# Performance work log

Hardware: AMD Instinct MI355X
Metric: run time of the kernel (lower is better)

The kernel has to match this reference:

```python
import jax, jax.numpy as jnp
import numpy as np

B, MAXLEN, H, T, NC = 2048, 1000, 512, 21, 10  # T = 21 one-hot classes -> seq_len


def _uniform(key, shape, bound):
    return jax.random.uniform(key, shape, jnp.float32, -bound, bound)


def setup_inputs() -> dict:
    key = jax.random.key(0)
    ks = jax.random.split(key, 16)
    k = 1.0 / np.sqrt(H)
    inp = {
        "x": jax.random.randint(ks[0], (B, MAXLEN), 0, 21),
        # layer 0: input size MAXLEN; stacked over 2 directions
        "w_ih0": _uniform(ks[1], (2, 4 * H, MAXLEN), k),
        "w_hh0": _uniform(ks[2], (2, 4 * H, H), k),
        "b_ih0": _uniform(ks[3], (2, 4 * H), k),
        "b_hh0": _uniform(ks[4], (2, 4 * H), k),
        # layer 1: input size 2H
        "w_ih1": _uniform(ks[5], (2, 4 * H, 2 * H), k),
        "w_hh1": _uniform(ks[6], (2, 4 * H, H), k),
        "b_ih1": _uniform(ks[7], (2, 4 * H), k),
        "b_hh1": _uniform(ks[8], (2, 4 * H), k),
        # emb: Linear(21 -> 1) over the seq axis
        "emb_w": _uniform(ks[9], (1, T), 1.0 / np.sqrt(T)),
        "emb_b": _uniform(ks[10], (1,), 1.0 / np.sqrt(T)),
        # fc: Linear(2H -> NC)
        "fc_w": _uniform(ks[11], (NC, 2 * H), 1.0 / np.sqrt(2 * H)),
        "fc_b": _uniform(ks[12], (NC,), 1.0 / np.sqrt(2 * H)),
    }
    return inp


def _lstm_dir(xs, w_ih, w_hh, b_ih, b_hh, reverse):
    # xs: [T, B, I]; PyTorch gate order i, f, g, o
    gx = jnp.einsum('tbi,gi->tbg', xs, w_ih) + b_ih + b_hh  # [T,B,4H]
    h_dim = w_hh.shape[1]
    bsz = xs.shape[1]

    def step(carry, g_t):
        h, c = carry
        g = g_t + h @ w_hh.T
        i, f, gg, o = jnp.split(g, 4, axis=-1)
        c = jax.nn.sigmoid(f) * c + jax.nn.sigmoid(i) * jnp.tanh(gg)
        h = jax.nn.sigmoid(o) * jnp.tanh(c)
        return (h, c), h

    init = (jnp.zeros((bsz, h_dim), xs.dtype), jnp.zeros((bsz, h_dim), xs.dtype))
    _, hs = jax.lax.scan(step, init, gx, reverse=reverse)
    return hs  # [T,B,H], time-aligned (matches torch bidirectional output)


def _bilstm_layer(xs, w_ih, w_hh, b_ih, b_hh):
    hf = _lstm_dir(xs, w_ih[0], w_hh[0], b_ih[0], b_hh[0], reverse=False)
    hb = _lstm_dir(xs, w_ih[1], w_hh[1], b_ih[1], b_hh[1], reverse=True)
    return jnp.concatenate([hf, hb], axis=-1)  # [T,B,2H]


def reference(x, w_ih0, w_hh0, b_ih0, b_hh0, w_ih1, w_hh1, b_ih1, b_hh1,
              emb_w, emb_b, fc_w, fc_b):
    xoh = jax.nn.one_hot(x, 21, dtype=jnp.float32)       # [B, MAXLEN, 21]
    seq = xoh.transpose(2, 0, 1)                          # [T=21, B, MAXLEN]
    seq = _bilstm_layer(seq, w_ih0, w_hh0, b_ih0, b_hh0)  # [T,B,2H]
    seq = _bilstm_layer(seq, w_ih1, w_hh1, b_ih1, b_hh1)  # [T,B,2H]
    # emb: Linear(21->1) applied along seq axis, then squeeze -> [B, 2H]
    z = jnp.einsum('tbh,t->bh', seq, emb_w[0]) + emb_b[0]
    return z @ fc_w.T + fc_b                              # [B, NC]
```

## Files before the change

### kernel.cpp

```cpp
#include <hip/hip_runtime.h>
#include <hip/hip_bf16.h>
#include <cstdint>
#include <cstddef>

#define B_SZ    2048
#define H_SZ    512
#define G4      2048
#define TSTEPS  21
#define MAXLEN  1000
#define KIN     1024
#define NCLS    10

#define BM    128
#define BN    128
#define BKS   32
#define LDSKS 40
#define NITS  16
#define NITG  32
#define GP2   68
#define STEPBUF (3 * BM * LDSKS)
#define GXBUF   (2 * BM * LDSKS)
#define SMEM_BYTES 61440

typedef short bf16x8 __attribute__((ext_vector_type(8)));
typedef float f32x4  __attribute__((ext_vector_type(4)));
typedef unsigned short ushort8 __attribute__((ext_vector_type(8)));

__device__ __forceinline__ unsigned short f2bf(float f) {
  __hip_bfloat16 h = __float2bfloat16(f);
  unsigned short u; __builtin_memcpy(&u, &h, sizeof(u)); return u;
}
__device__ __forceinline__ float bf2f(unsigned short u) {
  __hip_bfloat16 h; __builtin_memcpy(&h, &u, sizeof(h)); return __bfloat162float(h);
}
__device__ __forceinline__ float sigmoidf_(float x) {
  x = fminf(fmaxf(x, -30.f), 30.f);
  return 1.f / (1.f + __expf(-x));
}
__device__ __forceinline__ float tanhf_(float x) {
  float xc = fminf(fmaxf(x, -15.f), 15.f);
  float e = __expf(2.f * xc);
  return (e - 1.f) / (e + 1.f);
}
__device__ __forceinline__ void bar_lgkm() {
  asm volatile("s_waitcnt lgkmcnt(0)" ::: "memory");
  __builtin_amdgcn_s_barrier();
  __builtin_amdgcn_sched_barrier(0);
}
__device__ __forceinline__ int rbase_of(int p) { return (p & 3) * H_SZ + (p >> 2); }

__global__ void prep_rec_kernel(const float* __restrict__ w_hh,
                                unsigned short* __restrict__ Bhi,
                                unsigned short* __restrict__ Blo) {
  size_t idx = (size_t)blockIdx.x * blockDim.x + threadIdx.x;
  const size_t total = (size_t)2 * G4 * H_SZ;
  if (idx >= total) return;
  int k  = (int)(idx % H_SZ);
  size_t rowidx = idx / H_SZ;
  int p  = (int)(rowidx % G4);
  int dd = (int)(rowidx / G4);
  float w = w_hh[((size_t)dd * G4 + rbase_of(p)) * H_SZ + k];
  unsigned short h = f2bf(w);
  Bhi[idx] = h;
  Blo[idx] = f2bf(w - bf2f(h));
}

__global__ void prep_in0_kernel(const float* __restrict__ w_ih0,
                                unsigned short* __restrict__ Bin0) {
  size_t idx = (size_t)blockIdx.x * blockDim.x + threadIdx.x;
  const size_t total = (size_t)2 * G4 * KIN;
  if (idx >= total) return;
  int k  = (int)(idx % KIN);
  size_t rowidx = idx / KIN;
  int p  = (int)(rowidx % G4);
  int dd = (int)(rowidx / G4);
  float v = (k < MAXLEN) ? w_ih0[((size_t)dd * G4 + rbase_of(p)) * MAXLEN + k] : 0.f;
  Bin0[idx] = f2bf(v);
}

__global__ void prep_in1_kernel(const float* __restrict__ w_ih1,
                                unsigned short* __restrict__ Bin1) {
  size_t idx = (size_t)blockIdx.x * blockDim.x + threadIdx.x;
  const size_t total = (size_t)2 * G4 * KIN;
  if (idx >= total) return;
  int k  = (int)(idx % KIN);
  size_t rowidx = idx / KIN;
  int p  = (int)(rowidx % G4);
  int dd = (int)(rowidx / G4);
  Bin1[idx] = f2bf(w_ih1[((size_t)dd * G4 + rbase_of(p)) * KIN + k]);
}

__global__ void prep_b_kernel(const float* __restrict__ b_ih0,
                              const float* __restrict__ b_hh0,
                              const float* __restrict__ b_ih1,
                              const float* __restrict__ b_hh1,
                              float* __restrict__ bias0,
                              float* __restrict__ bias1) {
  int idx = blockIdx.x * blockDim.x + threadIdx.x;
  if (idx >= 2 * G4) return;
  int p  = idx % G4;
  int dd = idx / G4;
  int src = dd * G4 + rbase_of(p);
  bias0[idx] = b_ih0[src] + b_hh0[src];
  bias1[idx] = b_ih1[src] + b_hh1[src];
}

__global__ void prep_x_kernel(const int* __restrict__ x,
                              unsigned int* __restrict__ bits) {
  int idx = blockIdx.x * blockDim.x + threadIdx.x;
  if (idx >= B_SZ * 32) return;
  int b = idx >> 5;
  int w = idx & 31;
  const int* xr = x + (size_t)b * MAXLEN + w * 32;
  int xv[32];
#pragma unroll
  for (int j = 0; j < 32; ++j) {
    int k = w * 32 + j;
    xv[j] = (k < MAXLEN) ? xr[j] : -1;
  }
#pragma unroll
  for (int t = 0; t < TSTEPS; ++t) {
    unsigned int m = 0;
#pragma unroll
    for (int j = 0; j < 32; ++j)
      m |= (xv[j] == t) ? (1u << j) : 0u;
    bits[((size_t)t * B_SZ + b) * 32 + w] = m;
  }
}

template <int LAYER>
__device__ void step_role(char* smraw, int sid, int step,
                          const unsigned short* __restrict__ Bhrec,
                          const unsigned short* __restrict__ Blrec,
                          const float* __restrict__ bias,
                          const unsigned short* __restrict__ h_in,
                          unsigned short* __restrict__ h_out,
                          float* __restrict__ c_st,
                          unsigned short* __restrict__ seq_out,
                          float* __restrict__ zacc,
                          const float* __restrict__ emb_w,
                          const float* __restrict__ gxcur) {
  unsigned short* buf0 = (unsigned short*)smraw;
  unsigned short* buf1 = buf0 + STEPBUF;
  float*          gc   = (float*)smraw;

  const int tid  = threadIdx.x;
  const int lane = tid & 63;
  const int wave = tid >> 6;
  const int wr   = wave >> 1;
  const int wc   = wave & 1;
  const int q    = lane >> 4;
  const int r16  = lane & 15;

  const int xcd  = sid & 7;
  const int slot = sid >> 3;
  const int nb   = xcd * 2 + (slot & 1);
  const int mb   = (slot >> 1) & 15;
  const int d    = slot >> 5;
  const int tcur = d ? (TSTEPS - 1 - step) : step;
  const int n0   = nb * BN;
  const int m0   = mb * BM;

  const unsigned short* Bh_mat = Bhrec + (size_t)d * G4 * H_SZ;
  const unsigned short* Bl_mat = Blrec + (size_t)d * G4 * H_SZ;
  const unsigned short* Ah     = h_in + (size_t)d * B_SZ * H_SZ;

  float bval[4];
#pragma unroll
  for (int nt = 0; nt < 4; ++nt)
    bval[nt] = bias[d * G4 + n0 + wc * 64 + nt * 16 + r16];

  f32x4 acc[2][4];
#pragma unroll
  for (int mt = 0; mt < 2; ++mt)
#pragma unroll
    for (int nt = 0; nt < 4; ++nt) {
      f32x4 z = {0.f, 0.f, 0.f, 0.f};
      acc[mt][nt] = z;
    }

  const int rstg = tid >> 2;
  const int ostg = (tid & 3) * 8;

  ushort8 pbhA, pblA, pvaA, pbhB, pblB, pvaB;
  auto loadA = [&](int kt) {
    const int k0 = kt * BKS;
    pbhA = *(const ushort8*)(Bh_mat + (size_t)(n0 + rstg) * H_SZ + k0 + ostg);
    pblA = *(const ushort8*)(Bl_mat + (size_t)(n0 + rstg) * H_SZ + k0 + ostg);
    pvaA = *(const ushort8*)(Ah + (size_t)(m0 + rstg) * H_SZ + k0 + ostg);
  };
  auto loadB = [&](int kt) {
    const int k0 = kt * BKS;
    pbhB = *(const ushort8*)(Bh_mat + (size_t)(n0 + rstg) * H_SZ + k0 + ostg);
    pblB = *(const ushort8*)(Bl_mat + (size_t)(n0 + rstg) * H_SZ + k0 + ostg);
    pvaB = *(const ushort8*)(Ah + (size_t)(m0 + rstg) * H_SZ + k0 + ostg);
  };
  auto storeA = [&](unsigned short* sA) {
    *(ushort8*)(sA + rstg * LDSKS + ostg)                  = pvaA;
    *(ushort8*)(sA + BM * LDSKS + rstg * LDSKS + ostg)     = pbhA;
    *(ushort8*)(sA + 2 * BM * LDSKS + rstg * LDSKS + ostg) = pblA;
  };
  auto storeB = [&](unsigned short* sA) {
    *(ushort8*)(sA + rstg * LDSKS + ostg)                  = pvaB;
    *(ushort8*)(sA + BM * LDSKS + rstg * LDSKS + ostg)     = pbhB;
    *(ushort8*)(sA + 2 * BM * LDSKS + rstg * LDSKS + ostg) = pblB;
  };
  auto compute = [&](const unsigned short* sA) {
    const unsigned short* sBh = sA + BM * LDSKS;
    const unsigned short* sBl = sBh + BM * LDSKS;
    bf16x8 af[2], bh[4];
#pragma unroll
    for (int mt = 0; mt < 2; ++mt)
      af[mt] = *(const bf16x8*)(sA + (wr * 32 + mt * 16 + r16) * LDSKS + q * 8);
#pragma unroll
    for (int nt = 0; nt < 4; ++nt)
      bh[nt] = *(const bf16x8*)(sBh + (wc * 64 + nt * 16 + r16) * LDSKS + q * 8);
#pragma unroll
    for (int mt = 0; mt < 2; ++mt)
#pragma unroll
      for (int nt = 0; nt < 4; ++nt)
        acc[mt][nt] = __builtin_amdgcn_mfma_f32_16x16x32_bf16(af[mt], bh[nt], acc[mt][nt], 0, 0, 0);
    bf16x8 bl[4];
#pragma unroll
    for (int nt = 0; nt < 4; ++nt)
      bl[nt] = *(const bf16x8*)(sBl + (wc * 64 + nt * 16 + r16) * LDSKS + q * 8);
#pragma unroll
    for (int mt = 0; mt < 2; ++mt)
#pragma unroll
      for (int nt = 0; nt < 4; ++nt)
        acc[mt][nt] = __builtin_amdgcn_mfma_f32_16x16x32_bf16(af[mt], bl[nt], acc[mt][nt], 0, 0, 0);
  };

  float4 gpre[2][4];
  float  cpre[2][4];
  float  zpre[2][4];

  loadA(0);
  loadB(1);

  for (int kt2 = 0; kt2 < NITS; kt2 += 2) {
    storeA(buf0);
    bar_lgkm();
    if (kt2 + 2 < NITS) loadA(kt2 + 2);
    compute(buf0);

    storeB(buf1);
    bar_lgkm();
    if (kt2 + 3 < NITS) loadB(kt2 + 3);
    if (kt2 == NITS - 6) {
      const int jb = nb * 32;
#pragma unroll
      for (int cc = 0; cc < 2; ++cc)
#pragma unroll
        for (int it = 0; it < 4; ++it) {
          int cell = it * 512 + tid;
          int rl = cell >> 4, jq = cell & 15;
          int b = m0 + rl;
          int j = jb + cc * 16 + jq;
          gpre[cc][it] = *(const float4*)(gxcur + ((size_t)d * B_SZ + b) * G4 + (size_t)j * 4);
          cpre[cc][it] = c_st[((size_t)d * B_SZ + b) * H_SZ + j];
          if (LAYER == 1)
            zpre[cc][it] = zacc[(size_t)b * (2 * H_SZ) + d * H_SZ + j];
        }
    }
    compute(buf1);
  }
  __syncthreads();

  const int jbase = nb * 32;
  const float ew = (LAYER == 1) ? emb_w[tcur] : 0.f;

#pragma unroll
  for (int cc = 0; cc < 2; ++cc) {
    if (wc == cc) {
#pragma unroll
      for (int mt = 0; mt < 2; ++mt)
#pragma unroll
        for (int nt = 0; nt < 4; ++nt)
#pragma unroll
          for (int r = 0; r < 4; ++r) {
            int ml = wr * 32 + mt * 16 + q * 4 + r;
            gc[ml * GP2 + nt * 16 + r16] = acc[mt][nt][r] + bval[nt];
          }
    }
    __syncthreads();

#pragma unroll
    for (int it = 0; it < 4; ++it) {
      int cell = it * 512 + tid;
      int rl = cell >> 4, jq = cell & 15;
      int b = m0 + rl;
      int j = jbase + cc * 16 + jq;
      float4 g = *(const float4*)(&gc[rl * GP2 + jq * 4]);
      const float4 gx = gpre[cc][it];
      g.x += gx.x; g.y += gx.y; g.z += gx.z; g.w += gx.w;
      float si = sigmoidf_(g.x);
      float sf = sigmoidf_(g.y);
      float tg = tanhf_(g.z);
      float so = sigmoidf_(g.w);
      size_t cidx = ((size_t)d * B_SZ + b) * H_SZ + j;
      float cn = sf * cpre[cc][it] + si * tg;
      float hv = so * tanhf_(cn);
      c_st[cidx] = cn;
      h_out[cidx] = f2bf(hv);
      if (LAYER == 0) {
        seq_out[((size_t)tcur * B_SZ + b) * (2 * H_SZ) + d * H_SZ + j] = f2bf(hv);
      } else {
        zacc[(size_t)b * (2 * H_SZ) + d * H_SZ + j] = zpre[cc][it] + ew * hv;
      }
    }
    if (cc == 0) __syncthreads();
  }
}

template <int LAYER>
__device__ void gx_role(char* smraw, int gid, int gx_step,
                        const unsigned int* __restrict__ xbits,
                        const unsigned short* __restrict__ seq0,
                        const unsigned short* __restrict__ Bin,
                        float* __restrict__ gxnext) {
  if (gx_step >= TSTEPS) return;

  unsigned short* buf0 = (unsigned short*)smraw;
  unsigned short* buf1 = buf0 + GXBUF;

  const int tid  = threadIdx.x;
  const int lane = tid & 63;
  const int wave = tid >> 6;
  const int wr   = wave >> 1;
  const int wc   = wave & 1;
  const int q    = lane >> 4;
  const int r16  = lane & 15;

  const int xcd  = gid & 7;
  const int slot = gid >> 3;
  const int nb   = xcd * 2 + (slot & 1);
  const int mb   = (slot >> 1) & 15;
  const int d    = slot >> 5;
  const int tg   = d ? (TSTEPS - 1 - gx_step) : gx_step;
  const int n0   = nb * BN;
  const int m0   = mb * BM;

  const unsigned short* Bmat = Bin + (size_t)d * G4 * KIN;
  const unsigned char*  xrow = (const unsigned char*)xbits + ((size_t)tg * B_SZ) * (KIN / 8);
  const unsigned short* Asrc = seq0 + (size_t)tg * B_SZ * (2 * H_SZ);

  f32x4 acc[2][4];
#pragma unroll
  for (int mt = 0; mt < 2; ++mt)
#pragma unroll
    for (int nt = 0; nt < 4; ++nt) {
      f32x4 z = {0.f, 0.f, 0.f, 0.f};
      acc[mt][nt] = z;
    }

  const int rstg = tid >> 2;
  const int ostg = (tid & 3) * 8;

  ushort8 pbA, paA, pbB, paB;
  unsigned int bvA, bvB;
  auto loadA = [&](int kt) {
    const int k0 = kt * BKS;
    pbA = *(const ushort8*)(Bmat + (size_t)(n0 + rstg) * KIN + k0 + ostg);
    if (LAYER == 0) {
      bvA = xrow[(size_t)(m0 + rstg) * (KIN / 8) + (k0 + ostg) / 8];
    } else {
      paA = *(const ushort8*)(Asrc + (size_t)(m0 + rstg) * (2 * H_SZ) + k0 + ostg);
    }
  };
  auto loadB = [&](int kt) {
    const int k0 = kt * BKS;
    pbB = *(const ushort8*)(Bmat + (size_t)(n0 + rstg) * KIN + k0 + ostg);
    if (LAYER == 0) {
      bvB = xrow[(size_t)(m0 + rstg) * (KIN / 8) + (k0 + ostg) / 8];
    } else {
      paB = *(const ushort8*)(Asrc + (size_t)(m0 + rstg) * (2 * H_SZ) + k0 + ostg);
    }
  };
  auto expand = [&](unsigned int bv, unsigned short* sA) {
    unsigned int pk[4];
#pragma unroll
    for (int e = 0; e < 4; ++e) {
      pk[e] = (((bv >> (2 * e)) & 1u) ? 0x3F80u : 0u)
            | (((bv >> (2 * e + 1)) & 1u) ? 0x3F800000u : 0u);
    }
    *(uint4*)(sA + rstg * LDSKS + ostg) = make_uint4(pk[0], pk[1], pk[2], pk[3]);
  };
  auto storeA = [&](unsigned short* sA) {
    unsigned short* sB = sA + BM * LDSKS;
    if (LAYER == 0) expand(bvA, sA);
    else            *(ushort8*)(sA + rstg * LDSKS + ostg) = paA;
    *(ushort8*)(sB + rstg * LDSKS + ostg) = pbA;
  };
  auto storeB = [&](unsigned short* sA) {
    unsigned short* sB = sA + BM * LDSKS;
    if (LAYER == 0) expand(bvB, sA);
    else            *(ushort8*)(sA + rstg * LDSKS + ostg) = paB;
    *(ushort8*)(sB + rstg * LDSKS + ostg) = pbB;
  };
  auto compute = [&](const unsigned short* sA) {
    const unsigned short* sB = sA + BM * LDSKS;
    bf16x8 af[2], bh[4];
#pragma unroll
    for (int mt = 0; mt < 2; ++mt)
      af[mt] = *(const bf16x8*)(sA + (wr * 32 + mt * 16 + r16) * LDSKS + q * 8);
#pragma unroll
    for (int nt = 0; nt < 4; ++nt)
      bh[nt] = *(const bf16x8*)(sB + (wc * 64 + nt * 16 + r16) * LDSKS + q * 8);
#pragma unroll
    for (int mt = 0; mt < 2; ++mt)
#pragma unroll
      for (int nt = 0; nt < 4; ++nt)
        acc[mt][nt] = __builtin_amdgcn_mfma_f32_16x16x32_bf16(af[mt], bh[nt], acc[mt][nt], 0, 0, 0);
  };

  loadA(0);
  loadB(1);

  for (int kt2 = 0; kt2 < NITG; kt2 += 2) {
    storeA(buf0);
    bar_lgkm();
    if (kt2 + 2 < NITG) loadA(kt2 + 2);
    compute(buf0);

    storeB(buf1);
    bar_lgkm();
    if (kt2 + 3 < NITG) loadB(kt2 + 3);
    compute(buf1);
  }

#pragma unroll
  for (int mt = 0; mt < 2; ++mt)
#pragma unroll
    for (int nt = 0; nt < 4; ++nt)
#pragma unroll
      for (int r = 0; r < 4; ++r) {
        int row = m0 + wr * 32 + mt * 16 + q * 4 + r;
        int col = n0 + wc * 64 + nt * 16 + r16;
        gxnext[((size_t)d * B_SZ + row) * G4 + col] = acc[mt][nt][r];
      }
}

template <int LAYER>
__global__ __launch_bounds__(512, 4)
void fused_kernel(const unsigned int* __restrict__ xbits,
                  const unsigned short* __restrict__ seq0,
                  const unsigned short* __restrict__ Bin,
                  const unsigned short* __restrict__ Bhrec,
                  const unsigned short* __restrict__ Blrec,
                  const float* __restrict__ bias,
                  const unsigned short* __restrict__ h_in,
                  unsigned short* __restrict__ h_out,
                  float* __restrict__ c_st,
                  unsigned short* __restrict__ seq_out,
                  float* __restrict__ zacc,
                  const float* __restrict__ emb_w,
                  const float* __restrict__ gxcur,
                  float* __restrict__ gxnext,
                  int step, int gx_step) {
  extern __shared__ char smraw[];
  const int bid = blockIdx.x;
  if ((bid & 1) == 0) {
    step_role<LAYER>(smraw, bid >> 1, step, Bhrec, Blrec, bias, h_in, h_out,
                     c_st, seq_out, zacc, emb_w, gxcur);
  } else {
    gx_role<LAYER>(smraw, bid >> 1, gx_step, xbits, seq0, Bin, gxnext);
  }
}

template <int LAYER>
__global__ __launch_bounds__(512, 4)
void gx_only_kernel(const unsigned int* __restrict__ xbits,
                    const unsigned short* __restrict__ seq0,
                    const unsigned short* __restrict__ Bin,
                    float* __restrict__ gxnext, int gx_step) {
  extern __shared__ char smraw[];
  gx_role<LAYER>(smraw, blockIdx.x, gx_step, xbits, seq0, Bin, gxnext);
}

__global__ __launch_bounds__(256)
void final_kernel(const float* __restrict__ zacc,
                  const float* __restrict__ emb_b,
                  const float* __restrict__ fc_w,
                  const float* __restrict__ fc_b,
                  float* __restrict__ out) {
  const int b = blockIdx.x;
  const int tid = threadIdx.x;
  const int c0 = tid * 4;

  const float zb = emb_b[0];
  const float4 z4 = *(const float4*)(zacc + (size_t)b * (2 * H_SZ) + c0);
  float z0 = z4.x + zb, z1 = z4.y + zb, z2 = z4.z + zb, z3 = z4.w + zb;

  float part[NCLS];
#pragma unroll
  for (int nc = 0; nc < NCLS; ++nc) {
    const float4 f = *(const float4*)(fc_w + (size_t)nc * (2 * H_SZ) + c0);
    part[nc] = z0 * f.x + z1 * f.y + z2 * f.z + z3 * f.w;
  }
#pragma unroll
  for (int nc = 0; nc < NCLS; ++nc)
#pragma unroll
    for (int off2 = 32; off2 > 0; off2 >>= 1)
      part[nc] += __shfl_down(part[nc], off2);

  __shared__ float red[4][NCLS];
  if ((tid & 63) == 0) {
#pragma unroll
    for (int nc = 0; nc < NCLS; ++nc) red[tid >> 6][nc] = part[nc];
  }
  __syncthreads();
  if (tid < NCLS) {
    float s = red[0][tid] + red[1][tid] + red[2][tid] + red[3][tid] + fc_b[tid];
    out[b * NCLS + tid] = s;
  }
}

extern "C" void kernel_launch(void* const* d_in, const int* in_sizes, int n_in,
                              void* d_out, int out_size, void* d_ws, size_t ws_size,
                              hipStream_t stream) {
  (void)in_sizes; (void)n_in; (void)out_size; (void)ws_size;

  const int*   x     = (const int*)d_in[0];
  const float* w_ih0 = (const float*)d_in[1];
  const float* w_hh0 = (const float*)d_in[2];
  const float* b_ih0 = (const float*)d_in[3];
  const float* b_hh0 = (const float*)d_in[4];
  const float* w_ih1 = (const float*)d_in[5];
  const float* w_hh1 = (const float*)d_in[6];
  const float* b_ih1 = (const float*)d_in[7];
  const float* b_hh1 = (const float*)d_in[8];
  const float* emb_w = (const float*)d_in[9];
  const float* emb_b = (const float*)d_in[10];
  const float* fc_w  = (const float*)d_in[11];
  const float* fc_b  = (const float*)d_in[12];

  char* ws = (char*)d_ws;
  size_t off = 0;
  auto alloc = [&](size_t bytes) -> void* {
    void* p = ws + off;
    off += (bytes + 255) & ~(size_t)255;
    return p;
  };
  const size_t bin_b  = (size_t)2 * G4 * KIN * 2;
  const size_t brec_b = (size_t)2 * G4 * H_SZ * 2;
  const size_t xb_b   = (size_t)TSTEPS * B_SZ * 32 * 4;
  const size_t h_b    = (size_t)2 * B_SZ * H_SZ * 2;
  const size_t c_b    = (size_t)2 * B_SZ * H_SZ * 4;
  const size_t gx_b   = (size_t)2 * B_SZ * G4 * 4;
  const size_t seq_b  = (size_t)TSTEPS * B_SZ * (2 * H_SZ) * 2;
  const size_t z_b    = (size_t)B_SZ * (2 * H_SZ) * 4;

  unsigned short* Bin0  = (unsigned short*)alloc(bin_b);
  unsigned short* Bin1  = (unsigned short*)alloc(bin_b);
  unsigned short* Bh0   = (unsigned short*)alloc(brec_b);
  unsigned short* Bl0   = (unsigned short*)alloc(brec_b);
  unsigned short* Bh1   = (unsigned short*)alloc(brec_b);
  unsigned short* Bl1   = (unsigned short*)alloc(brec_b);
  float*          bias0 = (float*)alloc((size_t)2 * G4 * 4);
  float*          bias1 = (float*)alloc((size_t)2 * G4 * 4);
  unsigned int*   xbits = (unsigned int*)alloc(xb_b);
  unsigned short* hA    = (unsigned short*)alloc(h_b);
  unsigned short* hB    = (unsigned short*)alloc(h_b);
  float*          cst   = (float*)alloc(c_b);
  float*          gxA   = (float*)alloc(gx_b);
  float*          gxB   = (float*)alloc(gx_b);
  unsigned short* seq0  = (unsigned short*)alloc(seq_b);
  float*          zacc  = (float*)Bin0;

  {
    size_t ti = (size_t)2 * G4 * KIN;
    prep_in0_kernel<<<(int)((ti + 255) / 256), 256, 0, stream>>>(w_ih0, Bin0);
    prep_in1_kernel<<<(int)((ti + 255) / 256), 256, 0, stream>>>(w_ih1, Bin1);
    size_t tr = (size_t)2 * G4 * H_SZ;
    prep_rec_kernel<<<(int)((tr + 255) / 256), 256, 0, stream>>>(w_hh0, Bh0, Bl0);
    prep_rec_kernel<<<(int)((tr + 255) / 256), 256, 0, stream>>>(w_hh1, Bh1, Bl1);
    prep_b_kernel<<<16, 256, 0, stream>>>(b_ih0, b_hh0, b_ih1, b_hh1, bias0, bias1);
    prep_x_kernel<<<(B_SZ * 32 + 255) / 256, 256, 0, stream>>>(x, xbits);
  }

  hipMemsetAsync(hA, 0, h_b, stream);
  hipMemsetAsync(cst, 0, c_b, stream);
  gx_only_kernel<0><<<512, 512, SMEM_BYTES, stream>>>(xbits, nullptr, Bin0, gxA, 0);
  for (int s = 0; s < TSTEPS; ++s) {
    const unsigned short* hin  = (s & 1) ? hB : hA;
    unsigned short*       hout = (s & 1) ? hA : hB;
    float* cur = (s & 1) ? gxB : gxA;
    float* nxt = (s & 1) ? gxA : gxB;
    fused_kernel<0><<<1024, 512, SMEM_BYTES, stream>>>(
        xbits, nullptr, Bin0, Bh0, Bl0, bias0, hin, hout, cst,
        seq0, nullptr, nullptr, cur, nxt, s, s + 1);
  }

  hipMemsetAsync(hA, 0, h_b, stream);
  hipMemsetAsync(cst, 0, c_b, stream);
  hipMemsetAsync(zacc, 0, z_b, stream);
  gx_only_kernel<1><<<512, 512, SMEM_BYTES, stream>>>(nullptr, seq0, Bin1, gxA, 0);
  for (int s = 0; s < TSTEPS; ++s) {
    const unsigned short* hin  = (s & 1) ? hB : hA;
    unsigned short*       hout = (s & 1) ? hA : hB;
    float* cur = (s & 1) ? gxB : gxA;
    float* nxt = (s & 1) ? gxA : gxB;
    fused_kernel<1><<<1024, 512, SMEM_BYTES, stream>>>(
        nullptr, seq0, Bin1, Bh1, Bl1, bias1, hin, hout, cst,
        nullptr, zacc, emb_w, cur, nxt, s, s + 1);
  }

  final_kernel<<<B_SZ, 256, 0, stream>>>(zacc, emb_b, fc_w, fc_b, (float*)d_out);
}
```

Measured before the change: 2.682 ms.

## Halve block threads and give each wave a 64x64 MFMA tile

Block size drops from 512 to 256 threads while the 128x128 tile stays the same. Each wave now covers 64 rows instead of 32, with a 4x4 accumulator array, and each thread stages two rows per global load. The aim is more register-level reuse of the A and B fragments, since each LDS fragment read now feeds more MFMAs, and fewer waves contending for LDS and barriers. In exchange, register pressure rises, occupancy falls to two blocks per CU under the launch bounds, and the gx/c prefetch moves later in the K loop, so it has less time to hide latency.

Result: slower. 4.509 ms (+68.1%).

```diff
diff --git a/kernel.cpp b/kernel.cpp
--- a/kernel.cpp
+++ b/kernel.cpp
@@ -170,53 +170,70 @@
   for (int nt = 0; nt < 4; ++nt)
     bval[nt] = bias[d * G4 + n0 + wc * 64 + nt * 16 + r16];
 
-  f32x4 acc[2][4];
-#pragma unroll
-  for (int mt = 0; mt < 2; ++mt)
+  f32x4 acc[4][4];
+#pragma unroll
+  for (int mt = 0; mt < 4; ++mt)
 #pragma unroll
     for (int nt = 0; nt < 4; ++nt) {
       f32x4 z = {0.f, 0.f, 0.f, 0.f};
       acc[mt][nt] = z;
     }
 
-  const int rstg = tid >> 2;
-  const int ostg = (tid & 3) * 8;
-
-  ushort8 pbhA, pblA, pvaA, pbhB, pblB, pvaB;
+  const int ro = tid >> 2;
+  const int oo = (tid & 3) * 8;
+
+  ushort8 pbhA0, pbhA1, pblA0, pblA1, pvaA0, pvaA1;
+  ushort8 pbhB0, pbhB1, pblB0, pblB1, pvaB0, pvaB1;
   auto loadA = [&](int kt) {
     const int k0 = kt * BKS;
-    pbhA = *(const ushort8*)(Bh_mat + (size_t)(n0 + rstg) * H_SZ + k0 + ostg);
-    pblA = *(const ushort8*)(Bl_mat + (size_t)(n0 + rstg) * H_SZ + k0 + ostg);
-    pvaA = *(const ushort8*)(Ah + (size_t)(m0 + rstg) * H_SZ + k0 + ostg);
+    pbhA0 = *(const ushort8*)(Bh_mat + (size_t)(n0 + ro) * H_SZ + k0 + oo);
+    pbhA1 = *(const ushort8*)(Bh_mat + (size_t)(n0 + ro + 64) * H_SZ + k0 + oo);
+    pblA0 = *(const ushort8*)(Bl_mat + (size_t)(n0 + ro) * H_SZ + k0 + oo);
+    pblA1 = *(const ushort8*)(Bl_mat + (size_t)(n0 + ro + 64) * H_SZ + k0 + oo);
+    pvaA0 = *(const ushort8*)(Ah + (size_t)(m0 + ro) * H_SZ + k0 + oo);
+    pvaA1 = *(const ushort8*)(Ah + (size_t)(m0 + ro + 64) * H_SZ + k0 + oo);
   };
   auto loadB = [&](int kt) {
     const int k0 = kt * BKS;
-    pbhB = *(const ushort8*)(Bh_mat + (size_t)(n0 + rstg) * H_SZ + k0 + ostg);
-    pblB = *(const ushort8*)(Bl_mat + (size_t)(n0 + rstg) * H_SZ + k0 + ostg);
-    pvaB = *(const ushort8*)(Ah + (size_t)(m0 + rstg) * H_SZ + k0 + ostg);
+    pbhB0 = *(const ushort8*)(Bh_mat + (size_t)(n0 + ro) * H_SZ + k0 + oo);
+    pbhB1 = *(const ushort8*)(Bh_mat + (size_t)(n0 + ro + 64) * H_SZ + k0 + oo);
+    pblB0 = *(const ushort8*)(Bl_mat + (size_t)(n0 + ro) * H_SZ + k0 + oo);
+    pblB1 = *(const ushort8*)(Bl_mat + (size_t)(n0 + ro + 64) * H_SZ + k0 + oo);
+    pvaB0 = *(const ushort8*)(Ah + (size_t)(m0 + ro) * H_SZ + k0 + oo);
+    pvaB1 = *(const ushort8*)(Ah + (size_t)(m0 + ro + 64) * H_SZ + k0 + oo);
   };
   auto storeA = [&](unsigned short* sA) {
-    *(ushort8*)(sA + rstg * LDSKS + ostg)                  = pvaA;
-    *(ushort8*)(sA + BM * LDSKS + rstg * LDSKS + ostg)     = pbhA;
-    *(ushort8*)(sA + 2 * BM * LDSKS + rstg * LDSKS + ostg) = pblA;
+    unsigned short* sBh = sA + BM * LDSKS;
+    unsigned short* sBl = sBh + BM * LDSKS;
+    *(ushort8*)(sA + ro * LDSKS + oo)         = pvaA0;
+    *(ushort8*)(sA + (ro + 64) * LDSKS + oo)  = pvaA1;
+    *(ushort8*)(sBh + ro * LDSKS + oo)        = pbhA0;
+    *(ushort8*)(sBh + (ro + 64) * LDSKS + oo) = pbhA1;
+    *(ushort8*)(sBl + ro * LDSKS + oo)        = pblA0;
+    *(ushort8*)(sBl + (ro + 64) * LDSKS + oo) = pblA1;
   };
   auto storeB = [&](unsigned short* sA) {
-    *(ushort8*)(sA + rstg * LDSKS + ostg)                  = pvaB;
-    *(ushort8*)(sA + BM * LDSKS + rstg * LDSKS + ostg)     = pbhB;
-    *(ushort8*)(sA + 2 * BM * LDSKS + rstg * LDSKS + ostg) = pblB;
+    unsigned short* sBh = sA + BM * LDSKS;
+    unsigned short* sBl = sBh + BM * LDSKS;
+    *(ushort8*)(sA + ro * LDSKS + oo)         = pvaB0;
+    *(ushort8*)(sA + (ro + 64) * LDSKS + oo)  = pvaB1;
+    *(ushort8*)(sBh + ro * LDSKS + oo)        = pbhB0;
+    *(ushort8*)(sBh + (ro + 64) * LDSKS + oo) = pbhB1;
+    *(ushort8*)(sBl + ro * LDSKS + oo)        = pblB0;
+    *(ushort8*)(sBl + (ro + 64) * LDSKS + oo) = pblB1;
   };
   auto compute = [&](const unsigned short* sA) {
     const unsigned short* sBh = sA + BM * LDSKS;
     const unsigned short* sBl = sBh + BM * LDSKS;
-    bf16x8 af[2], bh[4];
-#pragma unroll
-    for (int mt = 0; mt < 2; ++mt)
-      af[mt] = *(const bf16x8*)(sA + (wr * 32 + mt * 16 + r16) * LDSKS + q * 8);
+    bf16x8 af[4], bh[4];
+#pragma unroll
+    for (int mt = 0; mt < 4; ++mt)
+      af[mt] = *(const bf16x8*)(sA + (wr * 64 + mt * 16 + r16) * LDSKS + q * 8);
 #pragma unroll
     for (int nt = 0; nt < 4; ++nt)
       bh[nt] = *(const bf16x8*)(sBh + (wc * 64 + nt * 16 + r16) * LDSKS + q * 8);
 #pragma unroll
-    for (int mt = 0; mt < 2; ++mt)
+    for (int mt = 0; mt < 4; ++mt)
 #pragma unroll
       for (int nt = 0; nt < 4; ++nt)
         acc[mt][nt] = __builtin_amdgcn_mfma_f32_16x16x32_bf16(af[mt], bh[nt], acc[mt][nt], 0, 0, 0);
@@ -225,15 +242,15 @@
     for (int nt = 0; nt < 4; ++nt)
       bl[nt] = *(const bf16x8*)(sBl + (wc * 64 + nt * 16 + r16) * LDSKS + q * 8);
 #pragma unroll
-    for (int mt = 0; mt < 2; ++mt)
+    for (int mt = 0; mt < 4; ++mt)
 #pragma unroll
       for (int nt = 0; nt < 4; ++nt)
         acc[mt][nt] = __builtin_amdgcn_mfma_f32_16x16x32_bf16(af[mt], bl[nt], acc[mt][nt], 0, 0, 0);
   };
 
-  float4 gpre[2][4];
-  float  cpre[2][4];
-  float  zpre[2][4];
+  float4 gpre[2][8];
+  float  cpre[2][8];
+  float  zpre[2][8];
 
   loadA(0);
   loadB(1);
@@ -247,13 +264,13 @@
     storeB(buf1);
     bar_lgkm();
     if (kt2 + 3 < NITS) loadB(kt2 + 3);
-    if (kt2 == NITS - 6) {
+    if (kt2 == NITS - 2) {
       const int jb = nb * 32;
 #pragma unroll
       for (int cc = 0; cc < 2; ++cc)
 #pragma unroll
-        for (int it = 0; it < 4; ++it) {
-          int cell = it * 512 + tid;
+        for (int it = 0; it < 8; ++it) {
+          int cell = it * 256 + tid;
           int rl = cell >> 4, jq = cell & 15;
           int b = m0 + rl;
           int j = jb + cc * 16 + jq;
@@ -274,20 +291,20 @@
   for (int cc = 0; cc < 2; ++cc) {
     if (wc == cc) {
 #pragma unroll
-      for (int mt = 0; mt < 2; ++mt)
+      for (int mt = 0; mt < 4; ++mt)
 #pragma unroll
         for (int nt = 0; nt < 4; ++nt)
 #pragma unroll
           for (int r = 0; r < 4; ++r) {
-            int ml = wr * 32 + mt * 16 + q * 4 + r;
+            int ml = wr * 64 + mt * 16 + q * 4 + r;
             gc[ml * GP2 + nt * 16 + r16] = acc[mt][nt][r] + bval[nt];
           }
     }
     __syncthreads();
 
 #pragma unroll
-    for (int it = 0; it < 4; ++it) {
-      int cell = it * 512 + tid;
+    for (int it = 0; it < 8; ++it) {
+      int cell = it * 256 + tid;
       int rl = cell >> 4, jq = cell & 15;
       int b = m0 + rl;
       int j = jbase + cc * 16 + jq;
@@ -345,70 +362,88 @@
   const unsigned char*  xrow = (const unsigned char*)xbits + ((size_t)tg * B_SZ) * (KIN / 8);
   const unsigned short* Asrc = seq0 + (size_t)tg * B_SZ * (2 * H_SZ);
 
-  f32x4 acc[2][4];
-#pragma unroll
-  for (int mt = 0; mt < 2; ++mt)
+  f32x4 acc[4][4];
+#pragma unroll
+  for (int mt = 0; mt < 4; ++mt)
 #pragma unroll
     for (int nt = 0; nt < 4; ++nt) {
       f32x4 z = {0.f, 0.f, 0.f, 0.f};
       acc[mt][nt] = z;
     }
 
-  const int rstg = tid >> 2;
-  const int ostg = (tid & 3) * 8;
-
-  ushort8 pbA, paA, pbB, paB;
-  unsigned int bvA, bvB;
+  const int ro = tid >> 2;
+  const int oo = (tid & 3) * 8;
+
+  ushort8 pbA0, pbA1, paA0, paA1, pbB0, pbB1, paB0, paB1;
+  unsigned int bvA0, bvA1, bvB0, bvB1;
   auto loadA = [&](int kt) {
     const int k0 = kt * BKS;
-    pbA = *(const ushort8*)(Bmat + (size_t)(n0 + rstg) * KIN + k0 + ostg);
+    pbA0 = *(const ushort8*)(Bmat + (size_t)(n0 + ro) * KIN + k0 + oo);
+    pbA1 = *(const ushort8*)(Bmat + (size_t)(n0 + ro + 64) * KIN + k0 + oo);
     if (LAYER == 0) {
-      bvA = xrow[(size_t)(m0 + rstg) * (KIN / 8) + (k0 + ostg) / 8];
+      bvA0 = xrow[(size_t)(m0 + ro) * (KIN / 8) + (k0 + oo) / 8];
+      bvA1 = xrow[(size_t)(m0 + ro + 64) * (KIN / 8) + (k0 + oo) / 8];
     } else {
-      paA = *(const ushort8*)(Asrc + (size_t)(m0 + rstg) * (2 * H_SZ) + k0 + ostg);
+      paA0 = *(const ushort8*)(Asrc + (size_t)(m0 + ro) * (2 * H_SZ) + k0 + oo);
+      paA1 = *(const ushort8*)(Asrc + (size_t)(m0 + ro + 64) * (2 * H_SZ) + k0 + oo);
     }
   };
   auto loadB = [&](int kt) {
     const int k0 = kt * BKS;
-    pbB = *(const ushort8*)(Bmat + (size_t)(n0 + rstg) * KIN + k0 + ostg);
+    pbB0 = *(const ushort8*)(Bmat + (size_t)(n0 + ro) * KIN + k0 + oo);
+    pbB1 = *(const ushort8*)(Bmat + (size_t)(n0 + ro + 64) * KIN + k0 + oo);
     if (LAYER == 0) {
-      bvB = xrow[(size_t)(m0 + rstg) * (KIN / 8) + (k0 + ostg) / 8];
+      bvB0 = xrow[(size_t)(m0 + ro) * (KIN / 8) + (k0 + oo) / 8];
+      bvB1 = xrow[(size_t)(m0 + ro + 64) * (KIN / 8) + (k0 + oo) / 8];
     } else {
-      paB = *(const ushort8*)(Asrc + (size_t)(m0 + rstg) * (2 * H_SZ) + k0 + ostg);
-    }
-  };
-  auto expand = [&](unsigned int bv, unsigned short* sA) {
+      paB0 = *(const ushort8*)(Asrc + (size_t)(m0 + ro) * (2 * H_SZ) + k0 + oo);
+      paB1 = *(const ushort8*)(Asrc + (size_t)(m0 + ro + 64) * (2 * H_SZ) + k0 + oo);
+    }
+  };
+  auto expand = [&](unsigned int bv, unsigned short* dst) {
     unsigned int pk[4];
 #pragma unroll
     for (int e = 0; e < 4; ++e) {
       pk[e] = (((bv >> (2 * e)) & 1u) ? 0x3F80u : 0u)
             | (((bv >> (2 * e + 1)) & 1u) ? 0x3F800000u : 0u);
     }
-    *(uint4*)(sA + rstg * LDSKS + ostg) = make_uint4(pk[0], pk[1], pk[2], pk[3]);
+    *(uint4*)dst = make_uint4(pk[0], pk[1], pk[2], pk[3]);
   };
   auto storeA = [&](unsigned short* sA) {
     unsigned short* sB = sA + BM * LDSKS;
-    if (LAYER == 0) expand(bvA, sA);
-    else            *(ushort8*)(sA + rstg * LDSKS + ostg) = paA;
-    *(ushort8*)(sB + rstg * LDSKS + ostg) = pbA;
+    if (LAYER == 0) {
+      expand(bvA0, sA + ro * LDSKS + oo);
+      expand(bvA1, sA + (ro + 64) * LDSKS + oo);
+    } else {
+      *(ushort8*)(sA + ro * LDSKS + oo)        = paA0;
+      *(ushort8*)(sA + (ro + 64) * LDSKS + oo) = paA1;
+    }
+    *(ushort8*)(sB + ro * LDSKS + oo)        = pbA0;
+    *(ushort8*)(sB + (ro + 64) * LDSKS + oo) = pbA1;
   };
   auto storeB = [&](unsigned short* sA) {
     unsigned short* sB = sA + BM * LDSKS;
-    if (LAYER == 0) expand(bvB, sA);
-    else            *(ushort8*)(sA + rstg * LDSKS + ostg) = paB;
-    *(ushort8*)(sB + rstg * LDSKS + ostg) = pbB;
+    if (LAYER == 0) {
+      expand(bvB0, sA + ro * LDSKS + oo);
+      expand(bvB1, sA + (ro + 64) * LDSKS + oo);
+    } else {
+      *(ushort8*)(sA + ro * LDSKS + oo)        = paB0;
+      *(ushort8*)(sA + (ro + 64) * LDSKS + oo) = paB1;
+    }
+    *(ushort8*)(sB + ro * LDSKS + oo)        = pbB0;
+    *(ushort8*)(sB + (ro + 64) * LDSKS + oo) = pbB1;
   };
   auto compute = [&](const unsigned short* sA) {
     const unsigned short* sB = sA + BM * LDSKS;
-    bf16x8 af[2], bh[4];
-#pragma unroll
-    for (int mt = 0; mt < 2; ++mt)
-      af[mt] = *(const bf16x8*)(sA + (wr * 32 + mt * 16 + r16) * LDSKS + q * 8);
+    bf16x8 af[4], bh[4];
+#pragma unroll
+    for (int mt = 0; mt < 4; ++mt)
+      af[mt] = *(const bf16x8*)(sA + (wr * 64 + mt * 16 + r16) * LDSKS + q * 8);
 #pragma unroll
     for (int nt = 0; nt < 4; ++nt)
       bh[nt] = *(const bf16x8*)(sB + (wc * 64 + nt * 16 + r16) * LDSKS + q * 8);
 #pragma unroll
-    for (int mt = 0; mt < 2; ++mt)
+    for (int mt = 0; mt < 4; ++mt)
 #pragma unroll
       for (int nt = 0; nt < 4; ++nt)
         acc[mt][nt] = __builtin_amdgcn_mfma_f32_16x16x32_bf16(af[mt], bh[nt], acc[mt][nt], 0, 0, 0);
@@ -430,19 +465,19 @@
   }
 
 #pragma unroll
-  for (int mt = 0; mt < 2; ++mt)
+  for (int mt = 0; mt < 4; ++mt)
 #pragma unroll
     for (int nt = 0; nt < 4; ++nt)
 #pragma unroll
       for (int r = 0; r < 4; ++r) {
-        int row = m0 + wr * 32 + mt * 16 + q * 4 + r;
+        int row = m0 + wr * 64 + mt * 16 + q * 4 + r;
         int col = n0 + wc * 64 + nt * 16 + r16;
         gxnext[((size_t)d * B_SZ + row) * G4 + col] = acc[mt][nt][r];
       }
 }
 
 template <int LAYER>
-__global__ __launch_bounds__(512, 4)
+__global__ __launch_bounds__(256, 2)
 void fused_kernel(const unsigned int* __restrict__ xbits,
                   const unsigned short* __restrict__ seq0,
                   const unsigned short* __restrict__ Bin,
@@ -469,7 +504,7 @@
 }
 
 template <int LAYER>
-__global__ __launch_bounds__(512, 4)
+__global__ __launch_bounds__(256, 2)
 void gx_only_kernel(const unsigned int* __restrict__ xbits,
                     const unsigned short* __restrict__ seq0,
                     const unsigned short* __restrict__ Bin,
@@ -581,13 +616,13 @@
 
   hipMemsetAsync(hA, 0, h_b, stream);
   hipMemsetAsync(cst, 0, c_b, stream);
-  gx_only_kernel<0><<<512, 512, SMEM_BYTES, stream>>>(xbits, nullptr, Bin0, gxA, 0);
+  gx_only_kernel<0><<<512, 256, SMEM_BYTES, stream>>>(xbits, nullptr, Bin0, gxA, 0);
   for (int s = 0; s < TSTEPS; ++s) {
     const unsigned short* hin  = (s & 1) ? hB : hA;
     unsigned short*       hout = (s & 1) ? hA : hB;
     float* cur = (s & 1) ? gxB : gxA;
     float* nxt = (s & 1) ? gxA : gxB;
-    fused_kernel<0><<<1024, 512, SMEM_BYTES, stream>>>(
+    fused_kernel<0><<<1024, 256, SMEM_BYTES, stream>>>(
         xbits, nullptr, Bin0, Bh0, Bl0, bias0, hin, hout, cst,
         seq0, nullptr, nullptr, cur, nxt, s, s + 1);
   }
@@ -595,13 +630,13 @@
   hipMemsetAsync(hA, 0, h_b, stream);
   hipMemsetAsync(cst, 0, c_b, stream);
   hipMemsetAsync(zacc, 0, z_b, stream);
-  gx_only_kernel<1><<<512, 512, SMEM_BYTES, stream>>>(nullptr, seq0, Bin1, gxA, 0);
+  gx_only_kernel<1><<<512, 256, SMEM_BYTES, stream>>>(nullptr, seq0, Bin1, gxA, 0);
   for (int s = 0; s < TSTEPS; ++s) {
     const unsigned short* hin  = (s & 1) ? hB : hA;
     unsigned short*       hout = (s & 1) ? hA : hB;
     float* cur = (s & 1) ? gxB : gxA;
     float* nxt = (s & 1) ? gxA : gxB;
-    fused_kernel<1><<<1024, 512, SMEM_BYTES, stream>>>(
+    fused_kernel<1><<<1024, 256, SMEM_BYTES, stream>>>(
         nullptr, seq0, Bin1, Bh1, Bl1, bias1, hin, hout, cst,
         nullptr, zacc, emb_w, cur, nxt, s, s + 1);
   }
```
